# Performance work log

Hardware: AMD Instinct MI355X
Metric: run time of the kernel (lower is better)

The kernel has to match this reference:

```python
import jax, jax.numpy as jnp
import numpy as np

B, L, H = 8, 512, 768
W = 5          # max_phrase_len
K = 32         # max_phrases
P = 256        # phrase_dim
EPS = 1e-5
NEG = -1e30


def layernorm(x, g, b):
    m = jnp.mean(x, axis=-1, keepdims=True)
    v = jnp.var(x, axis=-1, keepdims=True)
    return (x - m) * jax.lax.rsqrt(v + EPS) * g + b


def setup_inputs() -> dict:
    key = jax.random.key(0)
    ks = jax.random.split(key, 12)
    s = 0.02
    return {
        "hidden": jax.random.normal(ks[0], (B, L, H), dtype=jnp.float32),
        "attention_mask": jnp.ones((B, L), dtype=jnp.int32),
        # span_scorer: Linear(4H->H), LayerNorm(H), ReLU, Linear(H->1)
        "w1": jax.random.normal(ks[1], (4 * H, H), dtype=jnp.float32) * s,
        "b1": jnp.zeros((H,), dtype=jnp.float32),
        "g1": jnp.ones((H,), dtype=jnp.float32),
        "beta1": jnp.zeros((H,), dtype=jnp.float32),
        "w2": jax.random.normal(ks[2], (H, 1), dtype=jnp.float32) * s,
        "b2": jnp.zeros((1,), dtype=jnp.float32),
        # proj: Linear(H->P)
        "wp": jax.random.normal(ks[3], (H, P), dtype=jnp.float32) * s,
        "bp": jnp.zeros((P,), dtype=jnp.float32),
        # attention_gate: Linear(H->H/2), Tanh, Linear(H/2->1)
        "wg1": jax.random.normal(ks[4], (H, H // 2), dtype=jnp.float32) * s,
        "bg1": jnp.zeros((H // 2,), dtype=jnp.float32),
        "wg2": jax.random.normal(ks[5], (H // 2, 1), dtype=jnp.float32) * s,
        "bg2": jnp.zeros((1,), dtype=jnp.float32),
        # out_norm: LayerNorm(P)
        "gout": jnp.ones((P,), dtype=jnp.float32),
        "bout": jnp.zeros((P,), dtype=jnp.float32),
    }


def reference(hidden, attention_mask, w1, b1, g1, beta1, w2, b2,
              wp, bp, wg1, bg1, wg2, bg2, gout, bout):
    mask = attention_mask.astype(bool)  # [B,L]
    # validity of span (i, j=i+w): all tokens i..i+w in mask and i+w < L
    valids = []
    v = mask
    for w in range(W):
        if w > 0:
            shifted = jnp.pad(mask[:, w:], ((0, 0), (0, w)), constant_values=False)
            v = v & shifted
        valids.append(v)
    valid = jnp.stack(valids, axis=2)  # [B,L,W]

    # span means via prefix sums
    prefix = jnp.pad(jnp.cumsum(hidden, axis=1), ((0, 0), (1, 0), (0, 0)))  # [B,L+1,H]
    i_idx = jnp.arange(L)
    j_idx = jnp.minimum(i_idx[:, None] + jnp.arange(W)[None, :], L - 1)  # [L,W]

    start = hidden[:, :, None, :]                                  # [B,L,1,H]
    end = hidden[:, j_idx]                                         # [B,L,W,H]
    span_sum = prefix[:, j_idx + 1] - prefix[:, i_idx][:, :, None, :]
    mean = span_sum / (jnp.arange(W, dtype=hidden.dtype) + 1.0)[None, None, :, None]
    diff = end - start
    start_b = jnp.broadcast_to(start, end.shape)
    feat = jnp.concatenate([start_b, end, mean, diff], axis=-1)    # [B,L,W,4H]

    h = feat @ w1 + b1
    h = jax.nn.relu(layernorm(h, g1, beta1))                       # dropout is eval-mode identity
    score = (h @ w2 + b2)[..., 0]                                  # [B,L,W]
    score = jnp.where(valid, score, NEG)

    flat_scores = score.reshape(B, L * W)
    top_scores, top_idx = jax.lax.top_k(flat_scores, K)            # [B,K]
    phrase_masks = top_scores > NEG / 2

    mean_flat = mean.reshape(B, L * W, H)
    embs = jnp.take_along_axis(mean_flat, top_idx[..., None], axis=1)  # [B,K,H]
    embs = jnp.where(phrase_masks[..., None], embs, 0.0)               # zero-pad features
    phrase_scores = jnp.where(phrase_masks, top_scores, -10.0)

    ti = top_idx // W
    tw = top_idx % W
    spans = jnp.stack([ti, ti + tw], axis=-1)                      # [B,K,2]
    spans = jnp.where(phrase_masks[..., None], spans, 0)

    gate_logits = (jnp.tanh(embs @ wg1 + bg1) @ wg2 + bg2)[..., 0]  # [B,K]
    gate_logits = jnp.where(phrase_masks, gate_logits, -1e9)
    phrase_attention = jax.nn.softmax(gate_logits, axis=-1)

    phrase_embeds = layernorm(embs @ wp + bp, gout, bout)           # [B,K,P]
    return phrase_embeds, phrase_masks, phrase_attention, phrase_scores, spans
```

## Files before the change

kernel.cpp:

```cpp
#include <hip/hip_runtime.h>
#include <float.h>
#include <math.h>
#include <stdint.h>

#define B_   8
#define L_   512
#define H_   768
#define W_   5
#define K_   32
#define P_   256
#define EPS_ 1e-5f
#define NEG_ -1e30f

typedef _Float16 half8 __attribute__((ext_vector_type(8)));
typedef _Float16 half4v __attribute__((ext_vector_type(4)));
typedef float floatx4 __attribute__((ext_vector_type(4)));

static const size_t OFF_X   = 0;
static const size_t OFF_AH  = 9437184;
static const size_t OFF_AL  = 11010048;
static const size_t OFF_BH  = 12582912;
static const size_t OFF_BL  = 13467648;
static const size_t OFF_SC  = 14352384;
static const size_t OFF_TS  = 14372864;
static const size_t OFF_TI  = 14373120;
static const size_t OFF_GL  = 14373376;
static const size_t OFF_EMB = 14373632;
static const size_t OFF_Y   = 14570240;

#define A_SCALE 8.0f
#define B_SCALE 64.0f
#define INV_SCALE (1.0f / 512.0f)

__global__ __launch_bounds__(256) void prep_kernel(const float* __restrict__ hid,
                                                   const float* __restrict__ w1,
                                                   _Float16* __restrict__ ah,
                                                   _Float16* __restrict__ al,
                                                   _Float16* __restrict__ bh,
                                                   _Float16* __restrict__ bl) {
    __shared__ float ld[64][65];
    if (blockIdx.x < 3072) {
        int idx = (blockIdx.x * 256 + threadIdx.x) * 4;
        float4 x = *(const float4*)(hid + idx);
        float xs[4] = {x.x * A_SCALE, x.y * A_SCALE, x.z * A_SCALE, x.w * A_SCALE};
        half4v h, l;
#pragma unroll
        for (int i = 0; i < 4; ++i) {
            _Float16 hi = (_Float16)xs[i];
            h[i] = hi;
            l[i] = (_Float16)(xs[i] - (float)hi);
        }
        *(half4v*)(ah + idx) = h;
        *(half4v*)(al + idx) = l;
    } else {
        int bid = blockIdx.x - 3072;
        int n0 = (bid / 12) * 64;
        int k0 = (bid % 12) * 64;
        int t = threadIdx.x;
        int rsel = n0 / 768;
        int c0 = n0 - rsel * 768;
#pragma unroll 4
        for (int r = 0; r < 16; ++r) {
            int idx = r * 256 + t;
            int kk = idx >> 6, nn = idx & 63;
            int k = k0 + kk, c = c0 + nn;
            float v;
            if (rsel == 0)      v = w1[(size_t)k * 768 + c] - w1[(size_t)(2304 + k) * 768 + c];
            else if (rsel == 1) v = w1[(size_t)(768 + k) * 768 + c] + w1[(size_t)(2304 + k) * 768 + c];
            else                v = w1[(size_t)(1536 + k) * 768 + c];
            ld[kk][nn] = v * B_SCALE;
        }
        __syncthreads();
#pragma unroll 4
        for (int r = 0; r < 16; ++r) {
            int idx = r * 256 + t;
            int nn = idx >> 6, kk = idx & 63;
            float v = ld[kk][nn];
            _Float16 h = (_Float16)v;
            _Float16 lo = (_Float16)(v - (float)h);
            size_t o = (size_t)(n0 + nn) * 768 + k0 + kk;
            bh[o] = h;
            bl[o] = lo;
        }
    }
}

typedef const __attribute__((address_space(1))) void* gas_ptr;
typedef __attribute__((address_space(3))) void* las_ptr;
__device__ __forceinline__ void async_ld16(const _Float16* g, _Float16* l) {
    __builtin_amdgcn_global_load_lds((gas_ptr)g, (las_ptr)l, 16, 0, 0);
}

__global__ __launch_bounds__(256) void mfma_gemm_kernel(const _Float16* __restrict__ Ah,
                                                        const _Float16* __restrict__ Al,
                                                        const _Float16* __restrict__ Bh,
                                                        const _Float16* __restrict__ Bl,
                                                        float* __restrict__ C) {
    __shared__ _Float16 sAh[2 * 4096];
    __shared__ _Float16 sAl[2 * 4096];
    __shared__ _Float16 sBh[2 * 2048];
    __shared__ _Float16 sBl[2 * 2048];
    int tid = threadIdx.x;
    int lane = tid & 63;
    int wave = tid >> 6;
    int m0 = blockIdx.x * 128, n0 = blockIdx.y * 64;

    const _Float16* src = (wave == 0) ? Ah : (wave == 1) ? Al : (wave == 2) ? Bh : Bl;
    _Float16* dstb = (wave == 0) ? sAh : (wave == 1) ? sAl : (wave == 2) ? sBh : sBl;
    int psz  = (wave < 2) ? 4096 : 2048;
    int nch  = (wave < 2) ? 8 : 4;
    int row0 = (wave < 2) ? m0 : n0;
    int qg = (lane & 3) ^ ((lane >> 3) & 3);
    const _Float16* gp = src + (size_t)(row0 + (lane >> 2)) * 768 + qg * 8;

    int wr = wave >> 1, wc = wave & 1;
    int off_lane = (lane & 15) * 64 + (((lane >> 4) ^ ((lane >> 1) & 3)) * 16);
    floatx4 acc[4][2];
#pragma unroll
    for (int i = 0; i < 4; ++i)
#pragma unroll
        for (int j = 0; j < 2; ++j)
            acc[i][j] = (floatx4){0.f, 0.f, 0.f, 0.f};

#pragma unroll
    for (int c = 0; c < 8; ++c) {
        if (c < nch) async_ld16(gp + (size_t)c * 16 * 768, dstb + c * 512);
    }

    int parity = 0;
    for (int k0 = 0; k0 < 768; k0 += 32) {
        __syncthreads();
        if (k0 + 32 < 768) {
            _Float16* dst = dstb + (parity ^ 1) * psz;
            const _Float16* g = gp + k0 + 32;
#pragma unroll
            for (int c = 0; c < 8; ++c) {
                if (c < nch) async_ld16(g + (size_t)c * 16 * 768, dst + c * 512);
            }
        }

        const char* bAh = (const char*)sAh + parity * 8192 + wr * 4096 + off_lane;
        const char* bAl = (const char*)sAl + parity * 8192 + wr * 4096 + off_lane;
        const char* bBh = (const char*)sBh + parity * 4096 + wc * 2048 + off_lane;
        const char* bBl = (const char*)sBl + parity * 4096 + wc * 2048 + off_lane;
        half8 a_h[4], a_l[4], b_h[2], b_l[2];
#pragma unroll
        for (int i = 0; i < 4; ++i) {
            a_h[i] = *(const half8*)(bAh + i * 1024);
            a_l[i] = *(const half8*)(bAl + i * 1024);
        }
#pragma unroll
        for (int j = 0; j < 2; ++j) {
            b_h[j] = *(const half8*)(bBh + j * 1024);
            b_l[j] = *(const half8*)(bBl + j * 1024);
        }
#pragma unroll
        for (int i = 0; i < 4; ++i)
#pragma unroll
            for (int j = 0; j < 2; ++j) {
                acc[i][j] = __builtin_amdgcn_mfma_f32_16x16x32_f16(a_h[i], b_h[j], acc[i][j], 0, 0, 0);
                acc[i][j] = __builtin_amdgcn_mfma_f32_16x16x32_f16(a_h[i], b_l[j], acc[i][j], 0, 0, 0);
                acc[i][j] = __builtin_amdgcn_mfma_f32_16x16x32_f16(a_l[i], b_h[j], acc[i][j], 0, 0, 0);
            }
        parity ^= 1;
    }

    int colc = lane & 15, quad = lane >> 4;
#pragma unroll
    for (int i = 0; i < 4; ++i) {
#pragma unroll
        for (int r = 0; r < 4; ++r) {
            int row = m0 + wr * 64 + i * 16 + quad * 4 + r;
            float* Cp = C + (size_t)row * 2304 + n0 + wc * 32 + colc;
#pragma unroll
            for (int j = 0; j < 2; ++j)
                Cp[j * 16] = acc[i][j][r] * INV_SCALE;
        }
    }
}

__global__ __launch_bounds__(256) void score_kernel(const float* __restrict__ X,
                                                    const int* __restrict__ mask,
                                                    const float* __restrict__ b1,
                                                    const float* __restrict__ g1,
                                                    const float* __restrict__ beta1,
                                                    const float* __restrict__ w2,
                                                    const float* __restrict__ b2,
                                                    float* __restrict__ scores) {
    __shared__ float sE[8 * 768];
    __shared__ float sC[8 * 768];
    int tid = threadIdx.x;
    int wv = tid >> 6, lane = tid & 63;
    int bi0 = blockIdx.x * 4;
    int b = bi0 >> 9, i0 = bi0 & 511;

#pragma unroll
    for (int u0 = 0; u0 < 6; ++u0) {
        int u = u0 * 256 + tid;
        int t = u / 192, f = u - t * 192;
        int j = min(i0 + t, 511);
        const float4* Xj = (const float4*)(X + (size_t)(b * 512 + j) * 2304);
        ((float4*)sE)[t * 192 + f] = Xj[192 + f];
        ((float4*)sC)[t * 192 + f] = Xj[384 + f];
    }

    int i = i0 + wv, bi = bi0 + wv;
    float4 a[3], b1c[3], g1c[3], btc[3], w2c[3], ss[3];
    const float4* Xrow = (const float4*)(X + (size_t)bi * 2304);
#pragma unroll
    for (int q = 0; q < 3; ++q) {
        int f = lane + q * 64;
        a[q]   = Xrow[f];
        b1c[q] = ((const float4*)b1)[f];
        g1c[q] = ((const float4*)g1)[f];
        btc[q] = ((const float4*)beta1)[f];
        w2c[q] = ((const float4*)w2)[f];
        ss[q]  = make_float4(0.f, 0.f, 0.f, 0.f);
    }
    float bias2 = b2[0];
    __syncthreads();

    int jcur = i - 1;
    float4 e[3];
    float sc_loc[W_];

    for (int w = 0; w < W_; ++w) {
        int j = min(i + w, 511);
        if (j > jcur) {
            int slot = j - i0;
#pragma unroll
            for (int q = 0; q < 3; ++q) {
                int f = lane + q * 64;
                float4 cc = ((const float4*)sC)[slot * 192 + f];
                ss[q].x += cc.x; ss[q].y += cc.y; ss[q].z += cc.z; ss[q].w += cc.w;
                e[q] = ((const float4*)sE)[slot * 192 + f];
            }
            jcur = j;
        }
        float invw = 1.0f / (float)(w + 1);
        float4 h[3];
        float psum = 0.f, psq = 0.f;
#pragma unroll
        for (int q = 0; q < 3; ++q) {
            h[q].x = a[q].x + e[q].x + ss[q].x * invw + b1c[q].x;
            h[q].y = a[q].y + e[q].y + ss[q].y * invw + b1c[q].y;
            h[q].z = a[q].z + e[q].z + ss[q].z * invw + b1c[q].z;
            h[q].w = a[q].w + e[q].w + ss[q].w * invw + b1c[q].w;
            psum += h[q].x + h[q].y + h[q].z + h[q].w;
            psq  += h[q].x * h[q].x + h[q].y * h[q].y + h[q].z * h[q].z + h[q].w * h[q].w;
        }
#pragma unroll
        for (int m = 1; m < 64; m <<= 1) {
            psum += __shfl_xor(psum, m, 64);
            psq  += __shfl_xor(psq, m, 64);
        }
        float mean = psum * (1.f / 768.f);
        float var  = psq * (1.f / 768.f) - mean * mean;
        float rstd = rsqrtf(var + EPS_);

        float pd = 0.f;
#pragma unroll
        for (int q = 0; q < 3; ++q) {
            float yx = fmaxf((h[q].x - mean) * rstd * g1c[q].x + btc[q].x, 0.f);
            float yy = fmaxf((h[q].y - mean) * rstd * g1c[q].y + btc[q].y, 0.f);
            float yz = fmaxf((h[q].z - mean) * rstd * g1c[q].z + btc[q].z, 0.f);
            float yw = fmaxf((h[q].w - mean) * rstd * g1c[q].w + btc[q].w, 0.f);
            pd += yx * w2c[q].x + yy * w2c[q].y + yz * w2c[q].z + yw * w2c[q].w;
        }
#pragma unroll
        for (int m = 1; m < 64; m <<= 1) pd += __shfl_xor(pd, m, 64);
        sc_loc[w] = pd + bias2;
    }

    if (lane < W_) {
        int w = lane;
        bool ok = (i + w) < 512;
        if (ok) {
            for (int t = 0; t <= w; ++t) ok = ok && (mask[b * 512 + i + t] != 0);
        }
        scores[b * 2560 + i * 5 + w] = ok ? sc_loc[w] : NEG_;
    }
}

__device__ __forceinline__ uint64_t shfl_xor_u64(uint64_t x, int m) {
    uint32_t lo = (uint32_t)x, hi = (uint32_t)(x >> 32);
    lo = (uint32_t)__shfl_xor((int)lo, m, 64);
    hi = (uint32_t)__shfl_xor((int)hi, m, 64);
    return ((uint64_t)hi << 32) | lo;
}

__global__ __launch_bounds__(256) void topk_kernel(const float* __restrict__ scores,
                                                   float* __restrict__ tops,
                                                   int* __restrict__ topi,
                                                   float* __restrict__ out_masks,
                                                   float* __restrict__ out_scores,
                                                   float* __restrict__ out_spans) {
    int b = blockIdx.x;
    int tid = threadIdx.x;
    int lane = tid & 63;
    int wv = tid >> 6;
    __shared__ uint64_t lists[256 * 9];
    __shared__ uint64_t wmax[4];
    __shared__ uint64_t gS;

    uint64_t v[10];
#pragma unroll
    for (int q = 0; q < 10; ++q) {
        int t = q * 256 + tid;
        float f = scores[b * 2560 + t];
        uint32_t bits = __float_as_uint(f);
        uint32_t mk = bits ^ ((bits & 0x80000000u) ? 0xFFFFFFFFu : 0x80000000u);
        v[q] = ((uint64_t)mk << 32) | (uint64_t)(0xFFFFFFFFu - (uint32_t)t);
    }
#pragma unroll
    for (int p = 0; p < 5; ++p) {
#pragma unroll
        for (int i = 0; i < 9; i += 2) {
            if (v[i] < v[i + 1]) { uint64_t t = v[i]; v[i] = v[i + 1]; v[i + 1] = t; }
        }
#pragma unroll
        for (int i = 1; i < 9; i += 2) {
            if (v[i] < v[i + 1]) { uint64_t t = v[i]; v[i] = v[i + 1]; v[i + 1] = t; }
        }
    }
#pragma unroll
    for (int j = 0; j < 9; ++j) lists[tid * 9 + j] = v[j + 1];
    uint64_t my = v[0];
    int h = 0;

    for (int k = 0; k < K_; ++k) {
        uint64_t m = my;
#pragma unroll
        for (int s = 1; s < 64; s <<= 1) {
            uint64_t o = shfl_xor_u64(m, s);
            if (o > m) m = o;
        }
        if (lane == 0) wmax[wv] = m;
        __syncthreads();
        if (tid == 0) {
            uint64_t g = wmax[0];
#pragma unroll
            for (int q = 1; q < 4; ++q) if (wmax[q] > g) g = wmax[q];
            gS = g;
            uint32_t mk = (uint32_t)(g >> 32);
            uint32_t bits = mk ^ ((mk & 0x80000000u) ? 0x80000000u : 0xFFFFFFFFu);
            float tv = __uint_as_float(bits);
            int tix = (int)(0xFFFFFFFFu - (uint32_t)(g & 0xFFFFFFFFu));
            tops[b * 32 + k] = tv;
            topi[b * 32 + k] = tix;
            bool mm = tv > (NEG_ * 0.5f);
            out_masks[b * 32 + k] = mm ? 1.0f : 0.0f;
            out_scores[b * 32 + k] = mm ? tv : -10.0f;
            int tI = tix / 5, tw = tix % 5;
            out_spans[(b * 32 + k) * 2 + 0] = mm ? (float)tI : 0.0f;
            out_spans[(b * 32 + k) * 2 + 1] = mm ? (float)(tI + tw) : 0.0f;
        }
        __syncthreads();
        uint64_t g = gS;
        if (my == g) {
            my = (h < 9) ? lists[tid * 9 + h] : 0ull;
            ++h;
        }
    }
}

__global__ __launch_bounds__(256) void gather_emb_kernel(const float* __restrict__ hidden,
                                                         const float* __restrict__ tops,
                                                         const int* __restrict__ topi,
                                                         float* __restrict__ Embs) {
    int bk = blockIdx.x;
    int b = bk >> 5;
    int tid = threadIdx.x;
    int idx = topi[bk];
    bool valid = tops[bk] > (NEG_ * 0.5f);
    int tI = idx / 5, tw = idx % 5;
    int jend = min(tI + tw, L_ - 1);
    float inv = 1.0f / (float)(tw + 1);
#pragma unroll
    for (int q = 0; q < 3; ++q) {
        int c = tid + q * 256;
        float s = 0.f;
        if (valid) {
            for (int l = tI; l <= jend; ++l) s += hidden[(size_t)(b * 512 + l) * 768 + c];
            s *= inv;
        }
        Embs[(size_t)bk * 768 + c] = s;
    }
}

__global__ __launch_bounds__(256) void phrase_gemm_kernel(const float* __restrict__ Embs,
                                                          const float* __restrict__ wg1,
                                                          const float* __restrict__ bg1,
                                                          const float* __restrict__ wp,
                                                          const float* __restrict__ bp,
                                                          float* __restrict__ Y) {
    __shared__ float As[32][34];
    __shared__ float Bs[32][64];
    int tid = threadIdx.x;
    int m0 = blockIdx.x * 32;
    int cn0 = blockIdx.y * 64;
    const float* Wp; const float* biasp; int ldw;
    if (cn0 < 384) { Wp = wg1 + cn0;        biasp = bg1 + cn0;        ldw = 384; }
    else           { Wp = wp + (cn0 - 384); biasp = bp + (cn0 - 384); ldw = 256; }

    int tx = tid & 15;
    int ty = tid >> 4;
    int ar = tid >> 3, akq = (tid & 7) * 4;
    int bk = tid >> 3, bcq = (tid & 7) * 8;
    float acc[2][4] = {};

    for (int k0 = 0; k0 < 768; k0 += 32) {
        float4 av  = *(const float4*)(Embs + (size_t)(m0 + ar) * 768 + k0 + akq);
        float4 bv0 = *(const float4*)(Wp + (size_t)(k0 + bk) * ldw + bcq);
        float4 bv1 = *(const float4*)(Wp + (size_t)(k0 + bk) * ldw + bcq + 4);
        __syncthreads();
        As[akq + 0][ar] = av.x;
        As[akq + 1][ar] = av.y;
        As[akq + 2][ar] = av.z;
        As[akq + 3][ar] = av.w;
        *(float4*)&Bs[bk][bcq]     = bv0;
        *(float4*)&Bs[bk][bcq + 4] = bv1;
        __syncthreads();
#pragma unroll
        for (int kk = 0; kk < 32; ++kk) {
            float2 a = *(const float2*)&As[kk][ty * 2];
            float4 b = *(const float4*)&Bs[kk][tx * 4];
            acc[0][0] += a.x * b.x; acc[0][1] += a.x * b.y; acc[0][2] += a.x * b.z; acc[0][3] += a.x * b.w;
            acc[1][0] += a.y * b.x; acc[1][1] += a.y * b.y; acc[1][2] += a.y * b.z; acc[1][3] += a.y * b.w;
        }
    }
#pragma unroll
    for (int i = 0; i < 2; ++i) {
        float* Yp = Y + (size_t)(m0 + ty * 2 + i) * 640 + cn0 + tx * 4;
        float4 o = make_float4(acc[i][0] + biasp[tx * 4 + 0], acc[i][1] + biasp[tx * 4 + 1],
                               acc[i][2] + biasp[tx * 4 + 2], acc[i][3] + biasp[tx * 4 + 3]);
        *(float4*)Yp = o;
    }
}

__global__ __launch_bounds__(256) void phrase_post_kernel(const float* __restrict__ Y,
                                                          const float* __restrict__ wg2,
                                                          const float* __restrict__ bg2,
                                                          const float* __restrict__ tops,
                                                          const float* __restrict__ gout,
                                                          const float* __restrict__ bout,
                                                          float* __restrict__ gate,
                                                          float* __restrict__ out_embeds) {
    int wv = threadIdx.x >> 6, lane = threadIdx.x & 63;
    int row = blockIdx.x * 4 + wv;
    const float* Yrow = Y + (size_t)row * 640;

    float s = 0.f;
#pragma unroll
    for (int q = 0; q < 6; ++q) {
        int c = lane + q * 64;
        s += tanhf(Yrow[c]) * wg2[c];
    }
#pragma unroll
    for (int m = 1; m < 64; m <<= 1) s += __shfl_xor(s, m, 64);
    if (lane == 0) {
        bool valid = tops[row] > (NEG_ * 0.5f);
        gate[row] = valid ? (s + bg2[0]) : -1e9f;
    }

    float4 p = *(const float4*)(Yrow + 384 + lane * 4);
    float sm = p.x + p.y + p.z + p.w;
#pragma unroll
    for (int m = 1; m < 64; m <<= 1) sm += __shfl_xor(sm, m, 64);
    float mean = sm * (1.f / 256.f);
    float dx = p.x - mean, dy = p.y - mean, dz = p.z - mean, dw = p.w - mean;
    float v = dx * dx + dy * dy + dz * dz + dw * dw;
#pragma unroll
    for (int m = 1; m < 64; m <<= 1) v += __shfl_xor(v, m, 64);
    float rstd = rsqrtf(v * (1.f / 256.f) + EPS_);
    int c = lane * 4;
    float4 o;
    o.x = dx * rstd * gout[c]     + bout[c];
    o.y = dy * rstd * gout[c + 1] + bout[c + 1];
    o.z = dz * rstd * gout[c + 2] + bout[c + 2];
    o.w = dw * rstd * gout[c + 3] + bout[c + 3];
    *(float4*)(out_embeds + (size_t)row * 256 + c) = o;
}

__global__ void attn_kernel(const float* __restrict__ gate, float* __restrict__ out_attn) {
    int b = threadIdx.x;
    if (b < 8) {
        float mx = -FLT_MAX;
        for (int k = 0; k < 32; ++k) mx = fmaxf(mx, gate[b * 32 + k]);
        float e[32];
        float s = 0.f;
        for (int k = 0; k < 32; ++k) { e[k] = expf(gate[b * 32 + k] - mx); s += e[k]; }
        float inv = 1.f / s;
        for (int k = 0; k < 32; ++k) out_attn[b * 32 + k] = e[k] * inv;
    }
}

extern "C" void kernel_launch(void* const* d_in, const int* in_sizes, int n_in,
                              void* d_out, int out_size, void* d_ws, size_t ws_size,
                              hipStream_t stream) {
    const float* hidden = (const float*)d_in[0];
    const int*   amask  = (const int*)d_in[1];
    const float* w1     = (const float*)d_in[2];
    const float* b1     = (const float*)d_in[3];
    const float* g1     = (const float*)d_in[4];
    const float* beta1  = (const float*)d_in[5];
    const float* w2     = (const float*)d_in[6];
    const float* b2     = (const float*)d_in[7];
    const float* wp     = (const float*)d_in[8];
    const float* bp     = (const float*)d_in[9];
    const float* wg1    = (const float*)d_in[10];
    const float* bg1    = (const float*)d_in[11];
    const float* wg2    = (const float*)d_in[12];
    const float* bg2    = (const float*)d_in[13];
    const float* gout   = (const float*)d_in[14];
    const float* bout   = (const float*)d_in[15];

    float* ws = (float*)d_ws;
    float*     X    = ws + OFF_X;
    _Float16*  ah   = (_Float16*)(ws + OFF_AH);
    _Float16*  al   = (_Float16*)(ws + OFF_AL);
    _Float16*  bh   = (_Float16*)(ws + OFF_BH);
    _Float16*  bl   = (_Float16*)(ws + OFF_BL);
    float*     sc   = ws + OFF_SC;
    float*     ts   = ws + OFF_TS;
    int*       ti   = (int*)(ws + OFF_TI);
    float*     gl   = ws + OFF_GL;
    float*     Embs = ws + OFF_EMB;
    float*     Y    = ws + OFF_Y;

    float* out = (float*)d_out;
    float* out_embeds = out;
    float* out_masks  = out + 65536;
    float* out_attn   = out + 65792;
    float* out_scores = out + 66048;
    float* out_spans  = out + 66304;

    prep_kernel<<<3504, 256, 0, stream>>>(hidden, w1, ah, al, bh, bl);
    mfma_gemm_kernel<<<dim3(32, 36), 256, 0, stream>>>(ah, al, bh, bl, X);
    score_kernel<<<1024, 256, 0, stream>>>(X, amask, b1, g1, beta1, w2, b2, sc);
    topk_kernel<<<8, 256, 0, stream>>>(sc, ts, ti, out_masks, out_scores, out_spans);
    gather_emb_kernel<<<256, 256, 0, stream>>>(hidden, ts, ti, Embs);
    phrase_gemm_kernel<<<dim3(8, 10), 256, 0, stream>>>(Embs, wg1, bg1, wp, bp, Y);
    phrase_post_kernel<<<64, 256, 0, stream>>>(Y, wg2, bg2, ts, gout, bout, gl, out_embeds);
    attn_kernel<<<1, 64, 0, stream>>>(gl, out_attn);
}
```

Baseline: 233.5 us.

## Load GEMM B operand directly from global into registers, bypassing LDS

The B tiles (hi and lo halves) are no longer staged through shared memory. Each wave now loads its own B fragments straight from global memory into registers, one k-step ahead. All four waves now split the A-tile async LDS loads between them, and the k loop is fully unrolled. This drops the B LDS traffic and LDS footprint, at the cost of duplicated global B reads across the wr waves and more register pressure from prefetch buffers.

```diff
diff --git a/kernel.cpp b/kernel.cpp
--- a/kernel.cpp
+++ b/kernel.cpp
@@ -98,23 +98,23 @@
                                                         float* __restrict__ C) {
     __shared__ _Float16 sAh[2 * 4096];
     __shared__ _Float16 sAl[2 * 4096];
-    __shared__ _Float16 sBh[2 * 2048];
-    __shared__ _Float16 sBl[2 * 2048];
     int tid = threadIdx.x;
     int lane = tid & 63;
     int wave = tid >> 6;
     int m0 = blockIdx.x * 128, n0 = blockIdx.y * 64;
 
-    const _Float16* src = (wave == 0) ? Ah : (wave == 1) ? Al : (wave == 2) ? Bh : Bl;
-    _Float16* dstb = (wave == 0) ? sAh : (wave == 1) ? sAl : (wave == 2) ? sBh : sBl;
-    int psz  = (wave < 2) ? 4096 : 2048;
-    int nch  = (wave < 2) ? 8 : 4;
-    int row0 = (wave < 2) ? m0 : n0;
+    const _Float16* src = (wave < 2) ? Ah : Al;
+    _Float16* dstb = (wave < 2) ? sAh : sAl;
+    int co = (wave & 1) * 4;
     int qg = (lane & 3) ^ ((lane >> 3) & 3);
-    const _Float16* gp = src + (size_t)(row0 + (lane >> 2)) * 768 + qg * 8;
+    const _Float16* gp = src + (size_t)(m0 + co * 16 + (lane >> 2)) * 768 + qg * 8;
 
     int wr = wave >> 1, wc = wave & 1;
     int off_lane = (lane & 15) * 64 + (((lane >> 4) ^ ((lane >> 1) & 3)) * 16);
+
+    const _Float16* bhp = Bh + (size_t)(n0 + wc * 32 + (lane & 15)) * 768 + ((lane >> 4) * 8);
+    const _Float16* blp = Bl + (size_t)(n0 + wc * 32 + (lane & 15)) * 768 + ((lane >> 4) * 8);
+
     floatx4 acc[4][2];
 #pragma unroll
     for (int i = 0; i < 4; ++i)
@@ -123,36 +123,39 @@
             acc[i][j] = (floatx4){0.f, 0.f, 0.f, 0.f};
 
 #pragma unroll
-    for (int c = 0; c < 8; ++c) {
-        if (c < nch) async_ld16(gp + (size_t)c * 16 * 768, dstb + c * 512);
+    for (int c = 0; c < 4; ++c)
+        async_ld16(gp + (size_t)c * 16 * 768, dstb + (co + c) * 512);
+    half8 b_h[2], b_l[2], b_hn[2], b_ln[2];
+#pragma unroll
+    for (int j = 0; j < 2; ++j) {
+        b_h[j] = *(const half8*)(bhp + (size_t)j * 16 * 768);
+        b_l[j] = *(const half8*)(blp + (size_t)j * 16 * 768);
     }
 
     int parity = 0;
+#pragma unroll
     for (int k0 = 0; k0 < 768; k0 += 32) {
         __syncthreads();
         if (k0 + 32 < 768) {
-            _Float16* dst = dstb + (parity ^ 1) * psz;
+            _Float16* dst = dstb + (parity ^ 1) * 4096;
             const _Float16* g = gp + k0 + 32;
 #pragma unroll
-            for (int c = 0; c < 8; ++c) {
-                if (c < nch) async_ld16(g + (size_t)c * 16 * 768, dst + c * 512);
+            for (int c = 0; c < 4; ++c)
+                async_ld16(g + (size_t)c * 16 * 768, dst + (co + c) * 512);
+#pragma unroll
+            for (int j = 0; j < 2; ++j) {
+                b_hn[j] = *(const half8*)(bhp + (size_t)j * 16 * 768 + k0 + 32);
+                b_ln[j] = *(const half8*)(blp + (size_t)j * 16 * 768 + k0 + 32);
             }
         }
 
         const char* bAh = (const char*)sAh + parity * 8192 + wr * 4096 + off_lane;
         const char* bAl = (const char*)sAl + parity * 8192 + wr * 4096 + off_lane;
-        const char* bBh = (const char*)sBh + parity * 4096 + wc * 2048 + off_lane;
-        const char* bBl = (const char*)sBl + parity * 4096 + wc * 2048 + off_lane;
-        half8 a_h[4], a_l[4], b_h[2], b_l[2];
+        half8 a_h[4], a_l[4];
 #pragma unroll
         for (int i = 0; i < 4; ++i) {
             a_h[i] = *(const half8*)(bAh + i * 1024);
             a_l[i] = *(const half8*)(bAl + i * 1024);
-        }
-#pragma unroll
-        for (int j = 0; j < 2; ++j) {
-            b_h[j] = *(const half8*)(bBh + j * 1024);
-            b_l[j] = *(const half8*)(bBl + j * 1024);
         }
 #pragma unroll
         for (int i = 0; i < 4; ++i)
@@ -162,6 +165,11 @@
                 acc[i][j] = __builtin_amdgcn_mfma_f32_16x16x32_f16(a_h[i], b_l[j], acc[i][j], 0, 0, 0);
                 acc[i][j] = __builtin_amdgcn_mfma_f32_16x16x32_f16(a_l[i], b_h[j], acc[i][j], 0, 0, 0);
             }
+#pragma unroll
+        for (int j = 0; j < 2; ++j) {
+            b_h[j] = b_hn[j];
+            b_l[j] = b_ln[j];
+        }
         parity ^= 1;
     }
 
```

Result: slower. 258.3 us (+10.6%).
